# Optimization experiments

Hardware: AMD Instinct MI355X
Metric: run time of the kernel (lower is better)

## Reference

```python
import jax, jax.numpy as jnp
import numpy as np

B, E, R, A, NV, SEL = 512, 1024, 1024, 512, 196, 36

def _lstm_cell(x, h, c, Wih, bih, Whh, bhh):
    g = x @ Wih.T + bih + h @ Whh.T + bhh
    i, f, gg, o = jnp.split(g, 4, axis=1)  # torch gate order i,f,g,o
    c2 = jax.nn.sigmoid(f) * c + jax.nn.sigmoid(i) * jnp.tanh(gg)
    h2 = jax.nn.sigmoid(o) * jnp.tanh(c2)
    return h2, c2

def _attention(h, feats, p_feats, Wh, bh, Wa, ba):
    # feats: [B,S,R], p_feats: [B,S,A]
    att_h = h @ Wh.T + bh                       # [B,A]
    dot = jnp.tanh(p_feats + att_h[:, None, :])  # [B,S,A]
    scores = jnp.einsum('bsa,a->bs', dot, Wa[0]) + ba[0]
    w = jax.nn.softmax(scores, axis=1)
    return jnp.einsum('bs,bsd->bd', w, feats)

def setup_inputs() -> dict:
    key = jax.random.key(0)
    ks = jax.random.split(key, 32)
    s = 0.02
    inp = {
        'xt': jax.random.normal(ks[0], (B, E), jnp.float32),
        'fc_feats': jax.random.normal(ks[1], (B, R), jnp.float32),
        'att_feats': jax.random.normal(ks[2], (B, NV, R), jnp.float32),
        'p_att_feats': jax.random.normal(ks[3], (B, NV, A), jnp.float32),
        'state_h': jax.random.normal(ks[4], (2, B, R), jnp.float32),
        'state_c': jax.random.normal(ks[5], (2, B, R), jnp.float32),
        # att_lstm: input E + 2R
        'W_ih_att': jax.random.normal(ks[6], (4 * R, E + 2 * R), jnp.float32) * s,
        'b_ih_att': jnp.zeros((4 * R,), jnp.float32),
        'W_hh_att': jax.random.normal(ks[7], (4 * R, R), jnp.float32) * s,
        'b_hh_att': jnp.zeros((4 * R,), jnp.float32),
        # lang_lstm: input 3R
        'W_ih_lang': jax.random.normal(ks[8], (4 * R, 3 * R), jnp.float32) * s,
        'b_ih_lang': jnp.zeros((4 * R,), jnp.float32),
        'W_hh_lang': jax.random.normal(ks[9], (4 * R, R), jnp.float32) * s,
        'b_hh_lang': jnp.zeros((4 * R,), jnp.float32),
        # attention 1
        'Wh2att1': jax.random.normal(ks[10], (A, R), jnp.float32) * s,
        'bh2att1': jnp.zeros((A,), jnp.float32),
        'Walpha1': jax.random.normal(ks[11], (1, A), jnp.float32) * s,
        'balpha1': jnp.zeros((1,), jnp.float32),
        # vf attention
        'Wh2att2': jax.random.normal(ks[12], (A, R), jnp.float32) * s,
        'bh2att2': jnp.zeros((A,), jnp.float32),
        'Walpha2': jax.random.normal(ks[13], (1, A), jnp.float32) * s,
        'balpha2': jnp.zeros((1,), jnp.float32),
        # vf_layer and p_vf
        'W_vf': jax.random.normal(ks[14], (NV, 2 * R), jnp.float32) * s,
        'b_vf': jnp.zeros((NV,), jnp.float32),
        'W_pvf': jax.random.normal(ks[15], (A, R), jnp.float32) * s,
        'b_pvf': jnp.zeros((A,), jnp.float32),
    }
    return inp

def reference(xt, fc_feats, att_feats, p_att_feats, state_h, state_c,
              W_ih_att, b_ih_att, W_hh_att, b_hh_att,
              W_ih_lang, b_ih_lang, W_hh_lang, b_hh_lang,
              Wh2att1, bh2att1, Walpha1, balpha1,
              Wh2att2, bh2att2, Walpha2, balpha2,
              W_vf, b_vf, W_pvf, b_pvf):
    # dropout in eval mode -> identity
    prev_h = state_h[-1]
    att_lstm_input = jnp.concatenate([prev_h, fc_feats, xt], axis=1)
    h_att, c_att = _lstm_cell(att_lstm_input, state_h[0], state_c[0],
                              W_ih_att, b_ih_att, W_hh_att, b_hh_att)
    att = _attention(h_att, att_feats, p_att_feats, Wh2att1, bh2att1, Walpha1, balpha1)
    conc = jnp.concatenate([att, h_att], axis=1)          # [B,2R]
    vf_ha = conc @ W_vf.T + b_vf                          # [B,NV]
    vf_soft = jax.nn.softmax(vf_ha, axis=1)
    _, vf_ix = jax.lax.top_k(vf_soft, SEL)                # [B,SEL] (descending)
    arr1 = jnp.take_along_axis(att_feats, vf_ix[:, :, None], axis=1)  # [B,SEL,R]
    p_vf_feats = arr1 @ W_pvf.T + b_pvf                   # [B,SEL,A]
    vf_att = _attention(h_att, arr1, p_vf_feats, Wh2att2, bh2att2, Walpha2, balpha2)
    lang_lstm_input = jnp.concatenate([vf_att, h_att, att], axis=1)
    h_lang, c_lang = _lstm_cell(lang_lstm_input, state_h[1], state_c[1],
                                W_ih_lang, b_ih_lang, W_hh_lang, b_hh_lang)
    output = h_lang
    new_h = jnp.stack([h_att, h_lang])
    new_c = jnp.stack([c_att, c_lang])
    return output, new_h, new_c
```

## Files before the change

kernel.cpp:

```cpp
#include <hip/hip_runtime.h>

typedef __attribute__((ext_vector_type(4))) float f32x4;
typedef __attribute__((ext_vector_type(8))) _Float16 half8;
typedef __attribute__((ext_vector_type(4))) _Float16 half4;

__device__ __forceinline__ float fast_tanh(float x) {
  float e = __expf(2.f * x);
  return 1.f - 2.f / (e + 1.f);
}
__device__ __forceinline__ float fast_sigmoid(float x) {
  return 1.f / (1.f + __expf(-x));
}

__device__ __forceinline__ void gl_lds16(const _Float16* g, _Float16* l) {
  __builtin_amdgcn_global_load_lds(
      (const __attribute__((address_space(1))) void*)g,
      (__attribute__((address_space(3))) void*)l, 16, 0, 0);
}

template<int SPLIT, int OUT16, int NGUARD, int SWAPXY>
__global__ __launch_bounds__(256) void gemm16(
    const _Float16* __restrict__ Ahp, const _Float16* __restrict__ Alp, int lda,
    const _Float16* __restrict__ Bhp, const _Float16* __restrict__ Blp, int ldb,
    void* __restrict__ Cp, int ldc, long czstride,
    int N, int Kc)
{
  __shared__ _Float16 sAh[2][128 * 32];
  __shared__ _Float16 sBh[2][128 * 32];
  __shared__ _Float16 sAl[SPLIT == 3 ? 2 : 1][SPLIT == 3 ? 128 * 32 : 8];
  __shared__ _Float16 sBl[SPLIT == 3 ? 2 : 1][SPLIT == 3 ? 128 * 32 : 8];

  const int tid = threadIdx.x, lane = tid & 63, wid = tid >> 6;
  const int wm = wid >> 1, wn = wid & 1;
  const int l16 = lane & 15, k8 = lane >> 4;
  const int sr = lane >> 2;
  const int scol = ((lane & 3) ^ ((lane >> 3) & 3)) * 8;
  const int koff = ((k8 ^ ((lane >> 1) & 3))) * 8;

  const int  kt0   = blockIdx.z * Kc;
  const long abase = (long)(SWAPXY ? blockIdx.x : blockIdx.y) * 128;
  const long bbase = (long)(SWAPXY ? blockIdx.y : blockIdx.x) * 128;

  const int r0 = wid * 32 + sr;
  const int r1 = wid * 32 + 16 + sr;
  long br0 = bbase + r0, br1 = bbase + r1;
  if (NGUARD) {
    if (br0 > N - 1) br0 = N - 1;
    if (br1 > N - 1) br1 = N - 1;
  }

  const _Float16* ga0 = Ahp + (abase + r0) * (long)lda + kt0 + scol;
  const _Float16* ga1 = Ahp + (abase + r1) * (long)lda + kt0 + scol;
  const _Float16* gb0 = Bhp + br0 * (long)ldb + kt0 + scol;
  const _Float16* gb1 = Bhp + br1 * (long)ldb + kt0 + scol;
  const _Float16* la0 = SPLIT == 3 ? Alp + (abase + r0) * (long)lda + kt0 + scol : nullptr;
  const _Float16* la1 = SPLIT == 3 ? Alp + (abase + r1) * (long)lda + kt0 + scol : nullptr;
  const _Float16* lb0 = SPLIT == 3 ? Blp + br0 * (long)ldb + kt0 + scol : nullptr;
  const _Float16* lb1 = SPLIT == 3 ? Blp + br1 * (long)ldb + kt0 + scol : nullptr;

  const int e0 = (wid * 32) * 32;
  const int e1 = (wid * 32 + 16) * 32;

  f32x4 acc[4][4];
#pragma unroll
  for (int i = 0; i < 4; i++)
#pragma unroll
    for (int j = 0; j < 4; j++) acc[i][j] = (f32x4){0.f, 0.f, 0.f, 0.f};

  auto STAGE = [&](int buf, int kk) {
    gl_lds16(ga0 + kk, &sAh[buf][e0]);
    gl_lds16(ga1 + kk, &sAh[buf][e1]);
    gl_lds16(gb0 + kk, &sBh[buf][e0]);
    gl_lds16(gb1 + kk, &sBh[buf][e1]);
    if (SPLIT == 3) {
      gl_lds16(la0 + kk, &sAl[buf][e0]);
      gl_lds16(la1 + kk, &sAl[buf][e1]);
      gl_lds16(lb0 + kk, &sBl[buf][e0]);
      gl_lds16(lb1 + kk, &sBl[buf][e1]);
    }
  };

  STAGE(0, 0);

  const int nst = Kc >> 5;
  for (int t = 0; t < nst; t++) {
    const int buf = t & 1;
    if (t + 1 < nst) {
      STAGE(buf ^ 1, (t + 1) * 32);
      if (SPLIT == 3) asm volatile("s_waitcnt vmcnt(8)" ::: "memory");
      else            asm volatile("s_waitcnt vmcnt(4)" ::: "memory");
    } else {
      asm volatile("s_waitcnt vmcnt(0)" ::: "memory");
    }
    __builtin_amdgcn_sched_barrier(0);
    __builtin_amdgcn_s_barrier();
    __builtin_amdgcn_sched_barrier(0);

    half8 ah[4], bh[4];
#pragma unroll
    for (int m = 0; m < 4; m++)
      ah[m] = *(const half8*)&sAh[buf][(wm * 64 + m * 16 + l16) * 32 + koff];
#pragma unroll
    for (int n = 0; n < 4; n++)
      bh[n] = *(const half8*)&sBh[buf][(wn * 64 + n * 16 + l16) * 32 + koff];
#pragma unroll
    for (int m = 0; m < 4; m++)
#pragma unroll
      for (int n = 0; n < 4; n++)
        acc[m][n] = __builtin_amdgcn_mfma_f32_16x16x32_f16(ah[m], bh[n], acc[m][n], 0, 0, 0);
    if (SPLIT == 3) {
      half8 al[4], bl[4];
#pragma unroll
      for (int m = 0; m < 4; m++)
        al[m] = *(const half8*)&sAl[buf][(wm * 64 + m * 16 + l16) * 32 + koff];
#pragma unroll
      for (int n = 0; n < 4; n++)
        bl[n] = *(const half8*)&sBl[buf][(wn * 64 + n * 16 + l16) * 32 + koff];
#pragma unroll
      for (int m = 0; m < 4; m++)
#pragma unroll
        for (int n = 0; n < 4; n++) {
          acc[m][n] = __builtin_amdgcn_mfma_f32_16x16x32_f16(al[m], bh[n], acc[m][n], 0, 0, 0);
          acc[m][n] = __builtin_amdgcn_mfma_f32_16x16x32_f16(ah[m], bl[n], acc[m][n], 0, 0, 0);
        }
    }
    __builtin_amdgcn_sched_barrier(0);
    __builtin_amdgcn_s_barrier();
    __builtin_amdgcn_sched_barrier(0);
  }

  const long czoff = (long)blockIdx.z * czstride;
#pragma unroll
  for (int m = 0; m < 4; m++)
#pragma unroll
    for (int n = 0; n < 4; n++) {
      const long row0 = abase + wm * 64 + m * 16 + (lane >> 4) * 4;
      const long col  = bbase + wn * 64 + n * 16 + l16;
      if (!NGUARD || col < N) {
#pragma unroll
        for (int j = 0; j < 4; j++) {
          const long idx = (row0 + j) * (long)ldc + col + czoff;
          if (OUT16) ((_Float16*)Cp)[idx] = (_Float16)acc[m][n][j];
          else       ((float*)Cp)[idx] = acc[m][n][j];
        }
      }
    }
}

__global__ __launch_bounds__(256) void pack_kernel(
    const float* __restrict__ xt, const float* __restrict__ fc,
    const float* __restrict__ sh,
    _Float16* __restrict__ X1h, _Float16* __restrict__ X1l)
{
  int i = blockIdx.x * 256 + threadIdx.x;
  int b = i >> 10, rr = i & 1023;
  long base = (long)b * 4096;
  float v[4];
  v[0] = sh[524288 + i];
  v[1] = fc[i];
  v[2] = xt[i];
  v[3] = sh[i];
#pragma unroll
  for (int j = 0; j < 4; j++) {
    _Float16 h = (_Float16)v[j];
    X1h[base + j * 1024 + rr] = h;
    X1l[base + j * 1024 + rr] = (_Float16)(v[j] - (float)h);
  }
}

__global__ __launch_bounds__(256) void convertA_kernel(
    const float* __restrict__ WihA, const float* __restrict__ WhhA,
    const float* __restrict__ Wh1, const float* __restrict__ Wh2,
    const float* __restrict__ Wvf, const float* __restrict__ Wpvf,
    _Float16* __restrict__ WcAh, _Float16* __restrict__ WcAl,
    _Float16* __restrict__ W12h, _Float16* __restrict__ Wvfh,
    _Float16* __restrict__ Wvfl, _Float16* __restrict__ Wpvfh)
{
  int bi = blockIdx.x, t = threadIdx.x;
  if (bi < 16384) {
    long e = ((long)bi * 256 + t) * 4;
    int row = (int)(e >> 12), col = (int)(e & 4095);
    const float* src = (col < 3072) ? WihA + (long)row * 3072 + col
                                    : WhhA + (long)row * 1024 + (col - 3072);
    f32x4 v = *(const f32x4*)src;
    half4 h, l;
#pragma unroll
    for (int j = 0; j < 4; j++) { h[j] = (_Float16)v[j]; l[j] = (_Float16)(v[j] - (float)h[j]); }
    *(half4*)&WcAh[e] = h;
    *(half4*)&WcAl[e] = l;
  } else if (bi < 17408) {
    long e = ((long)(bi - 16384) * 256 + t) * 4;
    int row = (int)(e >> 10), col = (int)(e & 1023);
    const float* src = (row < 512) ? Wh1 + (long)row * 1024 + col
                                   : Wh2 + (long)(row - 512) * 1024 + col;
    f32x4 v = *(const f32x4*)src;
    half4 h;
#pragma unroll
    for (int j = 0; j < 4; j++) h[j] = (_Float16)v[j];
    *(half4*)&W12h[e] = h;
  } else if (bi < 17800) {
    long e = ((long)(bi - 17408) * 256 + t) * 4;
    f32x4 v = *(const f32x4*)(Wvf + e);
    half4 h, l;
#pragma unroll
    for (int j = 0; j < 4; j++) { h[j] = (_Float16)v[j]; l[j] = (_Float16)(v[j] - (float)h[j]); }
    *(half4*)&Wvfh[e] = h;
    *(half4*)&Wvfl[e] = l;
  } else {
    long e = ((long)(bi - 17800) * 256 + t) * 4;
    f32x4 v = *(const f32x4*)(Wpvf + e);
    half4 h;
#pragma unroll
    for (int j = 0; j < 4; j++) h[j] = (_Float16)v[j];
    *(half4*)&Wpvfh[e] = h;
  }
}

__global__ __launch_bounds__(256) void convertL_kernel(
    const float* __restrict__ WihL, const float* __restrict__ WhhL,
    _Float16* __restrict__ WcLh)
{
  long e = ((long)blockIdx.x * 256 + threadIdx.x) * 4;
  int row = (int)(e >> 12), col = (int)(e & 4095);
  const float* src = (col < 3072) ? WihL + (long)row * 3072 + col
                                  : WhhL + (long)row * 1024 + (col - 3072);
  f32x4 v = *(const f32x4*)src;
  half4 h;
#pragma unroll
  for (int j = 0; j < 4; j++) h[j] = (_Float16)v[j];
  *(half4*)&WcLh[e] = h;
}

template<int NP, bool H16, bool ATT>
__global__ __launch_bounds__(256) void lstm_act_kernel(
    const void* __restrict__ gp, const float* __restrict__ bih,
    const float* __restrict__ bhh, const float* __restrict__ cin,
    float* __restrict__ hOut, float* __restrict__ cOut,
    _Float16* __restrict__ hatt_h, _Float16* __restrict__ conch,
    _Float16* __restrict__ concl, _Float16* __restrict__ x2h,
    const float* __restrict__ sh, float* __restrict__ hOut2)
{
  const long S = 2097152;
  int i = blockIdx.x * 256 + threadIdx.x;
  int b = i >> 10, rr = i & 1023;
  long gb = (long)b * 4096;
  float g4[4];
#pragma unroll
  for (int q = 0; q < 4; q++) {
    float s = 0.f;
#pragma unroll
    for (int z = 0; z < NP; z++) {
      long off = (long)z * S + gb + q * 1024 + rr;
      s += H16 ? (float)((const _Float16*)gp)[off] : ((const float*)gp)[off];
    }
    g4[q] = s + bih[q * 1024 + rr] + bhh[q * 1024 + rr];
  }
  float c  = cin[i];
  float c2 = fast_sigmoid(g4[1]) * c + fast_sigmoid(g4[0]) * fast_tanh(g4[2]);
  float h2 = fast_sigmoid(g4[3]) * fast_tanh(c2);
  hOut[i] = h2;
  cOut[i] = c2;
  if (hOut2) hOut2[i] = h2;
  if (ATT) {
    _Float16 hh = (_Float16)h2;
    hatt_h[i] = hh;
    conch[(long)b * 2048 + 1024 + rr] = hh;
    concl[(long)b * 2048 + 1024 + rr] = (_Float16)(h2 - (float)hh);
    x2h[(long)b * 4096 + 1024 + rr] = hh;
    x2h[(long)b * 4096 + 3072 + rr] = (_Float16)sh[524288 + i];
  }
}

__global__ __launch_bounds__(256) void reduce_atth_kernel(
    const float* __restrict__ p, float* __restrict__ o)
{
  int i = (blockIdx.x * 256 + threadIdx.x) * 4;
  f32x4 a = *(const f32x4*)(p + i);
  f32x4 b = *(const f32x4*)(p + 524288 + i);
  f32x4 c = *(const f32x4*)(p + 1048576 + i);
  f32x4 d = *(const f32x4*)(p + 1572864 + i);
  *(f32x4*)(o + i) = a + b + c + d;
}

__global__ __launch_bounds__(256) void score1_kernel(
    const float* __restrict__ pf, const float* __restrict__ atth,
    const float* __restrict__ bh,
    const float* __restrict__ walpha, const float* __restrict__ balpha,
    float* __restrict__ out, int nrows)
{
  int gw = blockIdx.x * 4 + (threadIdx.x >> 6);
  int lane = threadIdx.x & 63;
  if (gw >= nrows) return;
  int b = gw / 196;
  const float* p  = pf + (long)gw * 512 + lane * 8;
  const float* ah = atth + (long)b * 1024 + lane * 8;
  const float* bp = bh + lane * 8;
  const float* wp = walpha + lane * 8;
  float acc = 0.f;
#pragma unroll
  for (int u = 0; u < 2; u++) {
    f32x4 pv = *(const f32x4*)(p + u * 4);
    f32x4 av = *(const f32x4*)(ah + u * 4);
    f32x4 bv = *(const f32x4*)(bp + u * 4);
    f32x4 wv = *(const f32x4*)(wp + u * 4);
#pragma unroll
    for (int j = 0; j < 4; j++)
      acc += fast_tanh(pv[j] + av[j] + bv[j]) * wv[j];
  }
#pragma unroll
  for (int off = 32; off; off >>= 1) acc += __shfl_xor(acc, off);
  if (lane == 0) out[gw] = acc + balpha[0];
}

__global__ __launch_bounds__(256) void attsum1_kernel(
    const float* __restrict__ scores, const float* __restrict__ feats,
    _Float16* __restrict__ conch, _Float16* __restrict__ concl, _Float16* __restrict__ x2h)
{
  __shared__ float w[256];
  int b = blockIdx.x, t = threadIdx.x;
  float s0 = (t < 196) ? scores[b * 196 + t] : -3.0e38f;
  w[t] = s0;
  __syncthreads();
  float mx = -3.0e38f;
  for (int i = 0; i < 196; i++) mx = fmaxf(mx, w[i]);
  float sum = 0.f;
  for (int i = 0; i < 196; i++) sum += __expf(w[i] - mx);
  float inv = 1.f / sum;
  __syncthreads();
  if (t < 196) w[t] = __expf(s0 - mx) * inv;
  __syncthreads();
  f32x4 acc = (f32x4){0.f, 0.f, 0.f, 0.f};
  const float* fb = feats + (long)b * 200704 + t * 4;
  for (int s0i = 0; s0i < 192; s0i += 8) {
    f32x4 v[8];
#pragma unroll
    for (int u = 0; u < 8; u++) v[u] = *(const f32x4*)(fb + (long)(s0i + u) * 1024);
#pragma unroll
    for (int u = 0; u < 8; u++) {
      float ws = w[s0i + u];
#pragma unroll
      for (int j = 0; j < 4; j++) acc[j] += ws * v[u][j];
    }
  }
#pragma unroll
  for (int u = 192; u < 196; u++) {
    float ws = w[u];
    f32x4 v = *(const f32x4*)(fb + (long)u * 1024);
#pragma unroll
    for (int j = 0; j < 4; j++) acc[j] += ws * v[j];
  }
  half4 h, l;
#pragma unroll
  for (int j = 0; j < 4; j++) { h[j] = (_Float16)acc[j]; l[j] = (_Float16)(acc[j] - (float)h[j]); }
  *(half4*)&conch[(long)b * 2048 + t * 4] = h;
  *(half4*)&concl[(long)b * 2048 + t * 4] = l;
  *(half4*)&x2h[(long)b * 4096 + 2048 + t * 4] = h;
}

__global__ __launch_bounds__(256) void vfatt_kernel(
    const _Float16* __restrict__ pvf16, const float* __restrict__ atth2,
    const float* __restrict__ bh2att2, const float* __restrict__ b_pvf,
    const float* __restrict__ walpha2, const float* __restrict__ balpha2,
    const _Float16* __restrict__ arr1h, _Float16* __restrict__ x2h)
{
  __shared__ float w[40];
  int b = blockIdx.x, tid = threadIdx.x;
  int lane = tid & 63, wv = tid >> 6;

  float add[8], wal[8];
#pragma unroll
  for (int u = 0; u < 8; u++) {
    int a = lane * 8 + u;
    add[u] = atth2[(long)b * 1024 + a] + bh2att2[a] + b_pvf[a];
    wal[u] = walpha2[a];
  }
  for (int j = wv; j < 36; j += 4) {
    half8 hv = *(const half8*)&pvf16[((long)b * 36 + j) * 512 + lane * 8];
    float acc = 0.f;
#pragma unroll
    for (int u = 0; u < 8; u++)
      acc += fast_tanh((float)hv[u] + add[u]) * wal[u];
#pragma unroll
    for (int off = 32; off; off >>= 1) acc += __shfl_xor(acc, off);
    if (lane == 0) w[j] = acc + balpha2[0];
  }
  __syncthreads();
  float mx = -3.0e38f;
  for (int i = 0; i < 36; i++) mx = fmaxf(mx, w[i]);
  float sum = 0.f;
  for (int i = 0; i < 36; i++) sum += __expf(w[i] - mx);
  float inv = 1.f / sum;
  __syncthreads();
  if (tid < 36) w[tid] = __expf(w[tid] - mx) * inv;
  __syncthreads();
  f32x4 acc = (f32x4){0.f, 0.f, 0.f, 0.f};
  const _Float16* fb = arr1h + (long)b * 36 * 1024 + tid * 4;
#pragma unroll 4
  for (int s = 0; s < 36; s++) {
    float ws = w[s];
    half4 v = *(const half4*)(fb + (long)s * 1024);
#pragma unroll
    for (int j = 0; j < 4; j++) acc[j] += ws * (float)v[j];
  }
  half4 h;
#pragma unroll
  for (int j = 0; j < 4; j++) h[j] = (_Float16)acc[j];
  *(half4*)&x2h[(long)b * 4096 + tid * 4] = h;
}

template<int NP>
__global__ __launch_bounds__(64) void topk_kernel(
    const float* __restrict__ vfp, const float* __restrict__ b_vf, int* __restrict__ ix)
{
  int b = blockIdx.x;
  int lane = threadIdx.x;
  float v[4];
#pragma unroll
  for (int j = 0; j < 4; j++) {
    int s = lane + 64 * j;
    float sum = -3.0e38f;
    if (s < 196) {
      sum = b_vf[s];
#pragma unroll
      for (int z = 0; z < NP; z++) sum += vfp[(long)z * 100352 + b * 196 + s];
    }
    v[j] = sum;
  }
  for (int it = 0; it < 36; it++) {
    float bv = -3.0e38f; int bs = 1 << 20;
#pragma unroll
    for (int j = 0; j < 4; j++) {
      int s = lane + 64 * j;
      if (v[j] > bv) { bv = v[j]; bs = s; }
    }
#pragma unroll
    for (int off = 32; off; off >>= 1) {
      float ov = __shfl_xor(bv, off);
      int   os = __shfl_xor(bs, off);
      if (ov > bv || (ov == bv && os < bs)) { bv = ov; bs = os; }
    }
    if ((bs & 63) == lane) v[bs >> 6] = -3.0e38f;
    if (lane == 0) ix[b * 36 + it] = bs;
  }
}

__global__ __launch_bounds__(256) void gather_conv_kernel(
    const float* __restrict__ feats, const int* __restrict__ ix, _Float16* __restrict__ dst)
{
  int bj = blockIdx.x;
  int b = bj / 36;
  int s = ix[bj];
  int t = threadIdx.x;
  f32x4 v = *(const f32x4*)(feats + ((long)b * 196 + s) * 1024 + t * 4);
  half4 h;
#pragma unroll
  for (int j = 0; j < 4; j++) h[j] = (_Float16)v[j];
  *(half4*)&dst[(long)bj * 1024 + t * 4] = h;
}

extern "C" void kernel_launch(void* const* d_in, const int* in_sizes, int n_in,
                              void* d_out, int out_size, void* d_ws, size_t ws_size,
                              hipStream_t stream) {
  const float* xt        = (const float*)d_in[0];
  const float* fc_feats  = (const float*)d_in[1];
  const float* att_feats = (const float*)d_in[2];
  const float* p_att     = (const float*)d_in[3];
  const float* state_h   = (const float*)d_in[4];
  const float* state_c   = (const float*)d_in[5];
  const float* b_ih_att  = (const float*)d_in[7];
  const float* b_hh_att  = (const float*)d_in[9];
  const float* b_ih_lang = (const float*)d_in[11];
  const float* b_hh_lang = (const float*)d_in[13];
  const float* bh2att1   = (const float*)d_in[15];
  const float* Walpha1   = (const float*)d_in[16];
  const float* balpha1   = (const float*)d_in[17];
  const float* bh2att2   = (const float*)d_in[19];
  const float* Walpha2   = (const float*)d_in[20];
  const float* balpha2   = (const float*)d_in[21];
  const float* b_vf      = (const float*)d_in[23];
  const float* b_pvf     = (const float*)d_in[25];

  float* out = (float*)d_out;
  float* W = (float*)d_ws;

  _Float16* WcAh   = (_Float16*)(W + 0);
  _Float16* WcAl   = (_Float16*)(W + 8388608);
  _Float16* WcLh   = (_Float16*)(W + 16777216);
  _Float16* X1h    = (_Float16*)(W + 25165824);
  _Float16* X1l    = (_Float16*)(W + 26214400);
  float*    g1p    = W + 27262976;
  _Float16* hatt_h = (_Float16*)(W + 35651584);
  _Float16* W12h   = (_Float16*)(W + 35913728);
  _Float16* Wvfh   = (_Float16*)(W + 36438016);
  _Float16* Wvfl   = (_Float16*)(W + 36638720);
  _Float16* Wpvfh  = (_Float16*)(W + 36839424);
  float*    atthp  = W + 37101568;
  float*    atth   = W + 39198720;
  _Float16* conch  = (_Float16*)(W + 39723008);
  _Float16* concl  = (_Float16*)(W + 40247296);
  _Float16* X2h    = (_Float16*)(W + 40771584);
  float*    scores1= W + 41820160;
  float*    vfhap  = W + 41920512;
  int*      vfix   = (int*)(W + 43526144);
  _Float16* arr1h  = (_Float16*)(W + 43544576);
  _Float16* pvf16  = (_Float16*)(W + 52981760);
  _Float16* g2ph   = (_Float16*)(W + 57700352);

  float* out_h0 = out + 524288;
  float* out_h1 = out + 2 * 524288;
  float* out_c0 = out + 3 * 524288;
  float* out_c1 = out + 4 * 524288;

  pack_kernel<<<2048, 256, 0, stream>>>(xt, fc_feats, state_h, X1h, X1l);

  convertA_kernel<<<18312, 256, 0, stream>>>(
      (const float*)d_in[6], (const float*)d_in[8],
      (const float*)d_in[14], (const float*)d_in[18],
      (const float*)d_in[22], (const float*)d_in[24],
      WcAh, WcAl, W12h, Wvfh, Wvfl, Wpvfh);

  gemm16<3, 0, 0, 0><<<dim3(32, 4, 4), 256, 0, stream>>>(
      X1h, X1l, 4096, WcAh, WcAl, 4096, g1p, 4096, 2097152, 4096, 1024);

  convertL_kernel<<<16384, 256, 0, stream>>>(
      (const float*)d_in[10], (const float*)d_in[12], WcLh);

  lstm_act_kernel<4, false, true><<<2048, 256, 0, stream>>>(
      g1p, b_ih_att, b_hh_att, state_c, out_h0, out_c0,
      hatt_h, conch, concl, X2h, state_h, nullptr);

  gemm16<1, 0, 0, 0><<<dim3(8, 4, 4), 256, 0, stream>>>(
      hatt_h, nullptr, 1024, W12h, nullptr, 1024, atthp, 1024, 524288, 1024, 256);
  reduce_atth_kernel<<<512, 256, 0, stream>>>(atthp, atth);

  score1_kernel<<<25088, 256, 0, stream>>>(
      p_att, atth, bh2att1, Walpha1, balpha1, scores1, 100352);

  attsum1_kernel<<<512, 256, 0, stream>>>(scores1, att_feats, conch, concl, X2h);

  gemm16<3, 0, 1, 0><<<dim3(2, 4, 16), 256, 0, stream>>>(
      conch, concl, 2048, Wvfh, Wvfl, 2048, vfhap, 196, 100352, 196, 128);

  topk_kernel<16><<<512, 64, 0, stream>>>(vfhap, b_vf, vfix);

  gather_conv_kernel<<<18432, 256, 0, stream>>>(att_feats, vfix, arr1h);

  gemm16<1, 1, 0, 1><<<dim3(144, 4, 1), 256, 0, stream>>>(
      arr1h, nullptr, 1024, Wpvfh, nullptr, 1024, pvf16, 512, 0, 512, 1024);

  vfatt_kernel<<<512, 256, 0, stream>>>(
      pvf16, atth + 512, bh2att2, b_pvf, Walpha2, balpha2, arr1h, X2h);

  gemm16<1, 1, 0, 0><<<dim3(32, 4, 4), 256, 0, stream>>>(
      X2h, nullptr, 4096, WcLh, nullptr, 4096, g2ph, 4096, 2097152, 4096, 1024);

  lstm_act_kernel<4, true, false><<<2048, 256, 0, stream>>>(
      g2ph, b_ih_lang, b_hh_lang, state_c + 524288, out, out_c1,
      nullptr, nullptr, nullptr, nullptr, nullptr, out_h1);
}
```

Baseline: 411.9 us.

## Merge prep kernels, fold atth split-K reduction into consumers, deepen lang GEMM split

```diff
diff --git a/kernel.cpp b/kernel.cpp
--- a/kernel.cpp
+++ b/kernel.cpp
@@ -19,7 +19,7 @@
 }
 
 template<int SPLIT, int OUT16, int NGUARD, int SWAPXY>
-__global__ __launch_bounds__(256) void gemm16(
+__global__ __launch_bounds__(256, SPLIT == 3 ? 2 : 4) void gemm16(
     const _Float16* __restrict__ Ahp, const _Float16* __restrict__ Alp, int lda,
     const _Float16* __restrict__ Bhp, const _Float16* __restrict__ Blp, int ldb,
     void* __restrict__ Cp, int ldc, long czstride,
@@ -147,34 +147,18 @@
     }
 }
 
-__global__ __launch_bounds__(256) void pack_kernel(
+__global__ __launch_bounds__(256) void prep_kernel(
+    const float* __restrict__ WihA, const float* __restrict__ WhhA,
+    const float* __restrict__ WihL, const float* __restrict__ WhhL,
+    const float* __restrict__ Wh1, const float* __restrict__ Wh2,
+    const float* __restrict__ Wvf, const float* __restrict__ Wpvf,
     const float* __restrict__ xt, const float* __restrict__ fc,
     const float* __restrict__ sh,
+    _Float16* __restrict__ WcAh, _Float16* __restrict__ WcAl,
+    _Float16* __restrict__ WcLh, _Float16* __restrict__ W12h,
+    _Float16* __restrict__ Wvfh, _Float16* __restrict__ Wvfl,
+    _Float16* __restrict__ Wpvfh,
     _Float16* __restrict__ X1h, _Float16* __restrict__ X1l)
-{
-  int i = blockIdx.x * 256 + threadIdx.x;
-  int b = i >> 10, rr = i & 1023;
-  long base = (long)b * 4096;
-  float v[4];
-  v[0] = sh[524288 + i];
-  v[1] = fc[i];
-  v[2] = xt[i];
-  v[3] = sh[i];
-#pragma unroll
-  for (int j = 0; j < 4; j++) {
-    _Float16 h = (_Float16)v[j];
-    X1h[base + j * 1024 + rr] = h;
-    X1l[base + j * 1024 + rr] = (_Float16)(v[j] - (float)h);
-  }
-}
-
-__global__ __launch_bounds__(256) void convertA_kernel(
-    const float* __restrict__ WihA, const float* __restrict__ WhhA,
-    const float* __restrict__ Wh1, const float* __restrict__ Wh2,
-    const float* __restrict__ Wvf, const float* __restrict__ Wpvf,
-    _Float16* __restrict__ WcAh, _Float16* __restrict__ WcAl,
-    _Float16* __restrict__ W12h, _Float16* __restrict__ Wvfh,
-    _Float16* __restrict__ Wvfl, _Float16* __restrict__ Wpvfh)
 {
   int bi = blockIdx.x, t = threadIdx.x;
   if (bi < 16384) {
@@ -188,8 +172,18 @@
     for (int j = 0; j < 4; j++) { h[j] = (_Float16)v[j]; l[j] = (_Float16)(v[j] - (float)h[j]); }
     *(half4*)&WcAh[e] = h;
     *(half4*)&WcAl[e] = l;
-  } else if (bi < 17408) {
+  } else if (bi < 32768) {
     long e = ((long)(bi - 16384) * 256 + t) * 4;
+    int row = (int)(e >> 12), col = (int)(e & 4095);
+    const float* src = (col < 3072) ? WihL + (long)row * 3072 + col
+                                    : WhhL + (long)row * 1024 + (col - 3072);
+    f32x4 v = *(const f32x4*)src;
+    half4 h;
+#pragma unroll
+    for (int j = 0; j < 4; j++) h[j] = (_Float16)v[j];
+    *(half4*)&WcLh[e] = h;
+  } else if (bi < 33792) {
+    long e = ((long)(bi - 32768) * 256 + t) * 4;
     int row = (int)(e >> 10), col = (int)(e & 1023);
     const float* src = (row < 512) ? Wh1 + (long)row * 1024 + col
                                    : Wh2 + (long)(row - 512) * 1024 + col;
@@ -198,37 +192,37 @@
 #pragma unroll
     for (int j = 0; j < 4; j++) h[j] = (_Float16)v[j];
     *(half4*)&W12h[e] = h;
-  } else if (bi < 17800) {
-    long e = ((long)(bi - 17408) * 256 + t) * 4;
+  } else if (bi < 34184) {
+    long e = ((long)(bi - 33792) * 256 + t) * 4;
     f32x4 v = *(const f32x4*)(Wvf + e);
     half4 h, l;
 #pragma unroll
     for (int j = 0; j < 4; j++) { h[j] = (_Float16)v[j]; l[j] = (_Float16)(v[j] - (float)h[j]); }
     *(half4*)&Wvfh[e] = h;
     *(half4*)&Wvfl[e] = l;
-  } else {
-    long e = ((long)(bi - 17800) * 256 + t) * 4;
+  } else if (bi < 34696) {
+    long e = ((long)(bi - 34184) * 256 + t) * 4;
     f32x4 v = *(const f32x4*)(Wpvf + e);
     half4 h;
 #pragma unroll
     for (int j = 0; j < 4; j++) h[j] = (_Float16)v[j];
     *(half4*)&Wpvfh[e] = h;
-  }
-}
-
-__global__ __launch_bounds__(256) void convertL_kernel(
-    const float* __restrict__ WihL, const float* __restrict__ WhhL,
-    _Float16* __restrict__ WcLh)
-{
-  long e = ((long)blockIdx.x * 256 + threadIdx.x) * 4;
-  int row = (int)(e >> 12), col = (int)(e & 4095);
-  const float* src = (col < 3072) ? WihL + (long)row * 3072 + col
-                                  : WhhL + (long)row * 1024 + (col - 3072);
-  f32x4 v = *(const f32x4*)src;
-  half4 h;
-#pragma unroll
-  for (int j = 0; j < 4; j++) h[j] = (_Float16)v[j];
-  *(half4*)&WcLh[e] = h;
+  } else {
+    int i = (bi - 34696) * 256 + t;
+    int b = i >> 10, rr = i & 1023;
+    long base = (long)b * 4096;
+    float v[4];
+    v[0] = sh[524288 + i];
+    v[1] = fc[i];
+    v[2] = xt[i];
+    v[3] = sh[i];
+#pragma unroll
+    for (int j = 0; j < 4; j++) {
+      _Float16 h = (_Float16)v[j];
+      X1h[base + j * 1024 + rr] = h;
+      X1l[base + j * 1024 + rr] = (_Float16)(v[j] - (float)h);
+    }
+  }
 }
 
 template<int NP, bool H16, bool ATT>
@@ -271,19 +265,8 @@
   }
 }
 
-__global__ __launch_bounds__(256) void reduce_atth_kernel(
-    const float* __restrict__ p, float* __restrict__ o)
-{
-  int i = (blockIdx.x * 256 + threadIdx.x) * 4;
-  f32x4 a = *(const f32x4*)(p + i);
-  f32x4 b = *(const f32x4*)(p + 524288 + i);
-  f32x4 c = *(const f32x4*)(p + 1048576 + i);
-  f32x4 d = *(const f32x4*)(p + 1572864 + i);
-  *(f32x4*)(o + i) = a + b + c + d;
-}
-
 __global__ __launch_bounds__(256) void score1_kernel(
-    const float* __restrict__ pf, const float* __restrict__ atth,
+    const float* __restrict__ pf, const float* __restrict__ atthp,
     const float* __restrict__ bh,
     const float* __restrict__ walpha, const float* __restrict__ balpha,
     float* __restrict__ out, int nrows)
@@ -293,19 +276,24 @@
   if (gw >= nrows) return;
   int b = gw / 196;
   const float* p  = pf + (long)gw * 512 + lane * 8;
-  const float* ah = atth + (long)b * 1024 + lane * 8;
   const float* bp = bh + lane * 8;
   const float* wp = walpha + lane * 8;
+  f32x4 av[2] = {(f32x4){0.f,0.f,0.f,0.f}, (f32x4){0.f,0.f,0.f,0.f}};
+#pragma unroll
+  for (int z = 0; z < 4; z++) {
+    const float* ap = atthp + (long)z * 524288 + (long)b * 1024 + lane * 8;
+    av[0] += *(const f32x4*)(ap);
+    av[1] += *(const f32x4*)(ap + 4);
+  }
   float acc = 0.f;
 #pragma unroll
   for (int u = 0; u < 2; u++) {
     f32x4 pv = *(const f32x4*)(p + u * 4);
-    f32x4 av = *(const f32x4*)(ah + u * 4);
     f32x4 bv = *(const f32x4*)(bp + u * 4);
     f32x4 wv = *(const f32x4*)(wp + u * 4);
 #pragma unroll
     for (int j = 0; j < 4; j++)
-      acc += fast_tanh(pv[j] + av[j] + bv[j]) * wv[j];
+      acc += fast_tanh(pv[j] + av[u][j] + bv[j]) * wv[j];
   }
 #pragma unroll
   for (int off = 32; off; off >>= 1) acc += __shfl_xor(acc, off);
@@ -358,7 +346,7 @@
 }
 
 __global__ __launch_bounds__(256) void vfatt_kernel(
-    const _Float16* __restrict__ pvf16, const float* __restrict__ atth2,
+    const _Float16* __restrict__ pvf16, const float* __restrict__ atthp,
     const float* __restrict__ bh2att2, const float* __restrict__ b_pvf,
     const float* __restrict__ walpha2, const float* __restrict__ balpha2,
     const _Float16* __restrict__ arr1h, _Float16* __restrict__ x2h)
@@ -371,8 +359,14 @@
 #pragma unroll
   for (int u = 0; u < 8; u++) {
     int a = lane * 8 + u;
-    add[u] = atth2[(long)b * 1024 + a] + bh2att2[a] + b_pvf[a];
+    add[u] = bh2att2[a] + b_pvf[a];
     wal[u] = walpha2[a];
+  }
+#pragma unroll
+  for (int z = 0; z < 4; z++) {
+    const float* ap = atthp + (long)z * 524288 + (long)b * 1024 + 512 + lane * 8;
+#pragma unroll
+    for (int u = 0; u < 8; u++) add[u] += ap[u];
   }
   for (int j = wv; j < 36; j += 4) {
     half8 hv = *(const half8*)&pvf16[((long)b * 36 + j) * 512 + lane * 8];
@@ -495,35 +489,31 @@
   _Float16* Wvfl   = (_Float16*)(W + 36638720);
   _Float16* Wpvfh  = (_Float16*)(W + 36839424);
   float*    atthp  = W + 37101568;
-  float*    atth   = W + 39198720;
-  _Float16* conch  = (_Float16*)(W + 39723008);
-  _Float16* concl  = (_Float16*)(W + 40247296);
-  _Float16* X2h    = (_Float16*)(W + 40771584);
-  float*    scores1= W + 41820160;
-  float*    vfhap  = W + 41920512;
-  int*      vfix   = (int*)(W + 43526144);
-  _Float16* arr1h  = (_Float16*)(W + 43544576);
-  _Float16* pvf16  = (_Float16*)(W + 52981760);
-  _Float16* g2ph   = (_Float16*)(W + 57700352);
+  _Float16* conch  = (_Float16*)(W + 39198720);
+  _Float16* concl  = (_Float16*)(W + 39723008);
+  _Float16* X2h    = (_Float16*)(W + 40247296);
+  float*    scores1= W + 41295872;
+  float*    vfhap  = W + 41396224;
+  int*      vfix   = (int*)(W + 43001856);
+  _Float16* arr1h  = (_Float16*)(W + 43020288);
+  _Float16* pvf16  = (_Float16*)(W + 52457472);
+  _Float16* g2ph   = (_Float16*)(W + 57176064);
 
   float* out_h0 = out + 524288;
   float* out_h1 = out + 2 * 524288;
   float* out_c0 = out + 3 * 524288;
   float* out_c1 = out + 4 * 524288;
 
-  pack_kernel<<<2048, 256, 0, stream>>>(xt, fc_feats, state_h, X1h, X1l);
-
-  convertA_kernel<<<18312, 256, 0, stream>>>(
+  prep_kernel<<<36744, 256, 0, stream>>>(
       (const float*)d_in[6], (const float*)d_in[8],
+      (const float*)d_in[10], (const float*)d_in[12],
       (const float*)d_in[14], (const float*)d_in[18],
       (const float*)d_in[22], (const float*)d_in[24],
-      WcAh, WcAl, W12h, Wvfh, Wvfl, Wpvfh);
+      xt, fc_feats, state_h,
+      WcAh, WcAl, WcLh, W12h, Wvfh, Wvfl, Wpvfh, X1h, X1l);
 
   gemm16<3, 0, 0, 0><<<dim3(32, 4, 4), 256, 0, stream>>>(
       X1h, X1l, 4096, WcAh, WcAl, 4096, g1p, 4096, 2097152, 4096, 1024);
-
-  convertL_kernel<<<16384, 256, 0, stream>>>(
-      (const float*)d_in[10], (const float*)d_in[12], WcLh);
 
   lstm_act_kernel<4, false, true><<<2048, 256, 0, stream>>>(
       g1p, b_ih_att, b_hh_att, state_c, out_h0, out_c0,
@@ -531,10 +521,9 @@
 
   gemm16<1, 0, 0, 0><<<dim3(8, 4, 4), 256, 0, stream>>>(
       hatt_h, nullptr, 1024, W12h, nullptr, 1024, atthp, 1024, 524288, 1024, 256);
-  reduce_atth_kernel<<<512, 256, 0, stream>>>(atthp, atth);
 
   score1_kernel<<<25088, 256, 0, stream>>>(
-      p_att, atth, bh2att1, Walpha1, balpha1, scores1, 100352);
+      p_att, atthp, bh2att1, Walpha1, balpha1, scores1, 100352);
 
   attsum1_kernel<<<512, 256, 0, stream>>>(scores1, att_feats, conch, concl, X2h);
 
@@ -549,12 +538,12 @@
       arr1h, nullptr, 1024, Wpvfh, nullptr, 1024, pvf16, 512, 0, 512, 1024);
 
   vfatt_kernel<<<512, 256, 0, stream>>>(
-      pvf16, atth + 512, bh2att2, b_pvf, Walpha2, balpha2, arr1h, X2h);
-
-  gemm16<1, 1, 0, 0><<<dim3(32, 4, 4), 256, 0, stream>>>(
-      X2h, nullptr, 4096, WcLh, nullptr, 4096, g2ph, 4096, 2097152, 4096, 1024);
-
-  lstm_act_kernel<4, true, false><<<2048, 256, 0, stream>>>(
+      pvf16, atthp, bh2att2, b_pvf, Walpha2, balpha2, arr1h, X2h);
+
+  gemm16<1, 1, 0, 0><<<dim3(32, 4, 8), 256, 0, stream>>>(
+      X2h, nullptr, 4096, WcLh, nullptr, 4096, g2ph, 4096, 2097152, 4096, 512);
+
+  lstm_act_kernel<8, true, false><<<2048, 256, 0, stream>>>(
       g2ph, b_ih_lang, b_hh_lang, state_c + 524288, out, out_c1,
       nullptr, nullptr, nullptr, nullptr, nullptr, out_h1);
 }
```

Result: slower. 425.4 us (+3.3%).
